# Optimization experiments

Hardware: AMD Instinct MI355X
Metric: run time of the kernel (lower is better)

## Reference

```python
import jax, jax.numpy as jnp
import numpy as np
from jax import lax

TAU = 0.1
DT = 0.001
UNITS = 1024
B, T = 16, 2048


def setup_inputs() -> dict:
    key = jax.random.key(0)
    inputs = jax.random.normal(key, (B, T, UNITS), dtype=jnp.float32)
    level_var = jnp.zeros((1, UNITS), dtype=jnp.float32)
    e = np.exp(-DT / TAU)
    smoothing_init = np.log(e / (1.0 - e)).astype(np.float32)
    smoothing_var = jnp.ones((1, UNITS), dtype=jnp.float32) * smoothing_init
    return {"inputs": inputs, "level_var": level_var, "smoothing_var": smoothing_var}


def reference(inputs, level_var, smoothing_var):
    # inputs: [B, T, U]; level_var, smoothing_var: [1, U]
    s = jax.nn.sigmoid(smoothing_var)  # [1, U]
    level0 = jnp.broadcast_to(level_var, (inputs.shape[0], inputs.shape[2]))  # [B, U]

    def step(level, x_t):
        new = (1.0 - s) * x_t + s * level  # [B, U]
        return new, new

    _, levels = lax.scan(step, level0, jnp.swapaxes(inputs, 0, 1))  # [T, B, U]
    return jnp.swapaxes(levels, 0, 1)  # [B, T, U]
```

## Files before the change

kernel.cpp:

```cpp
#include <hip/hip_runtime.h>


typedef float f32x4 __attribute__((ext_vector_type(4)));

constexpr int B   = 16;
constexpr int T   = 2048;
constexpr int U   = 1024;
constexpr int U4  = U / 4;
constexpr int BU4 = B * U4;

__device__ __forceinline__ float sigmoidf(float x) {
    return 1.0f / (1.0f + __expf(-x));
}

template <int C>
__global__ __launch_bounds__(64) void lowpass_partial(
    const f32x4* __restrict__ in,
    const float* __restrict__ smooth,
    f32x4*       __restrict__ P)
{
    constexpr int L  = T / C;
    constexpr int D1 = 16;
    static_assert(L > D1 && L % D1 == 0, "prefetch");

    const int tid = blockIdx.x * 64 + (int)threadIdx.x;
    const int c   = tid >> 12;
    const int lg  = tid & (BU4 - 1);
    const int b   = lg >> 8;
    const int ug  = lg & (U4 - 1);

    const f32x4 sm = reinterpret_cast<const f32x4*>(smooth)[ug];
    const float s0 = sigmoidf(sm.x), s1 = sigmoidf(sm.y),
                s2 = sigmoidf(sm.z), s3 = sigmoidf(sm.w);
    const float o0 = 1.0f - s0, o1 = 1.0f - s1,
                o2 = 1.0f - s2, o3 = 1.0f - s3;

    const f32x4* __restrict__ ip = in + (b * T + c * L) * U4 + ug;

    float a0 = 0.0f, a1 = 0.0f, a2 = 0.0f, a3 = 0.0f;
    f32x4 buf[D1];
    #pragma unroll
    for (int i = 0; i < D1; ++i) buf[i] = ip[i * U4];

    int t = 0;
    for (; t < L - D1; t += D1) {
        #pragma unroll
        for (int j = 0; j < D1; ++j) {
            f32x4 x = buf[j];
            buf[j] = ip[(t + D1 + j) * U4];
            a0 = fmaf(s0, a0, o0 * x.x);
            a1 = fmaf(s1, a1, o1 * x.y);
            a2 = fmaf(s2, a2, o2 * x.z);
            a3 = fmaf(s3, a3, o3 * x.w);
        }
    }
    #pragma unroll
    for (int j = 0; j < D1; ++j) {
        f32x4 x = buf[j];
        a0 = fmaf(s0, a0, o0 * x.x);
        a1 = fmaf(s1, a1, o1 * x.y);
        a2 = fmaf(s2, a2, o2 * x.z);
        a3 = fmaf(s3, a3, o3 * x.w);
    }
    f32x4 part; part.x = a0; part.y = a1; part.z = a2; part.w = a3;
    P[c * BU4 + lg] = part;
}

template <int C>
__global__ __launch_bounds__(64) void lowpass_scan(
    const f32x4* __restrict__ in,
    const float* __restrict__ level0,
    const float* __restrict__ smooth,
    const f32x4* __restrict__ P,
    f32x4*       __restrict__ out)
{
    constexpr int L    = T / C;
    constexpr int D2   = 8;
    constexpr int LOG2L = 31 - __builtin_clz(L);
    static_assert(L > D2 && L % D2 == 0, "prefetch");
    static_assert((1 << LOG2L) == L, "pow2");

    const int tid = blockIdx.x * 64 + (int)threadIdx.x;
    const int c   = tid >> 12;
    const int lg  = tid & (BU4 - 1);
    const int b   = lg >> 8;
    const int ug  = lg & (U4 - 1);

    const f32x4 sm = reinterpret_cast<const f32x4*>(smooth)[ug];
    const float s0 = sigmoidf(sm.x), s1 = sigmoidf(sm.y),
                s2 = sigmoidf(sm.z), s3 = sigmoidf(sm.w);
    const float o0 = 1.0f - s0, o1 = 1.0f - s1,
                o2 = 1.0f - s2, o3 = 1.0f - s3;

    float sL0 = s0, sL1 = s1, sL2 = s2, sL3 = s3;
    #pragma unroll
    for (int i = 0; i < LOG2L; ++i) {
        sL0 *= sL0; sL1 *= sL1; sL2 *= sL2; sL3 *= sL3;
    }

    const f32x4 l0 = reinterpret_cast<const f32x4*>(level0)[ug];
    float v0 = l0.x, v1 = l0.y, v2 = l0.z, v3 = l0.w;
    for (int i = 0; i < c; ++i) {
        f32x4 p = P[i * BU4 + lg];
        v0 = fmaf(sL0, v0, p.x);
        v1 = fmaf(sL1, v1, p.y);
        v2 = fmaf(sL2, v2, p.z);
        v3 = fmaf(sL3, v3, p.w);
    }

    const int base = (b * T + c * L) * U4 + ug;
    const f32x4* __restrict__ ip = in  + base;
    f32x4*       __restrict__ op = out + base;

    f32x4 buf[D2];
    #pragma unroll
    for (int i = 0; i < D2; ++i) buf[i] = ip[i * U4];

    int t = 0;
    for (; t < L - D2; t += D2) {
        #pragma unroll
        for (int j = 0; j < D2; ++j) {
            f32x4 x = buf[j];
            buf[j] = ip[(t + D2 + j) * U4];
            v0 = fmaf(s0, v0, o0 * x.x);
            v1 = fmaf(s1, v1, o1 * x.y);
            v2 = fmaf(s2, v2, o2 * x.z);
            v3 = fmaf(s3, v3, o3 * x.w);
            f32x4 r; r.x = v0; r.y = v1; r.z = v2; r.w = v3;
            __builtin_nontemporal_store(r, &op[(t + j) * U4]);
        }
    }
    #pragma unroll
    for (int j = 0; j < D2; ++j) {
        f32x4 x = buf[j];
        v0 = fmaf(s0, v0, o0 * x.x);
        v1 = fmaf(s1, v1, o1 * x.y);
        v2 = fmaf(s2, v2, o2 * x.z);
        v3 = fmaf(s3, v3, o3 * x.w);
        f32x4 r; r.x = v0; r.y = v1; r.z = v2; r.w = v3;
        __builtin_nontemporal_store(r, &op[(t + j) * U4]);
    }
}

extern "C" void kernel_launch(void* const* d_in, const int* in_sizes, int n_in,
                              void* d_out, int out_size, void* d_ws, size_t ws_size,
                              hipStream_t stream) {
    const f32x4* in     = (const f32x4*)d_in[0];
    const float* level0 = (const float*)d_in[1];
    const float* smooth = (const float*)d_in[2];
    f32x4* out          = (f32x4*)d_out;
    f32x4* P            = (f32x4*)d_ws;

    dim3 block(64);
    if (ws_size >= (size_t)16 * BU4 * sizeof(f32x4)) {
        constexpr int C = 16;
        dim3 grid(C * BU4 / 64);
        hipLaunchKernelGGL(lowpass_partial<C>, grid, block, 0, stream, in, smooth, P);
        hipLaunchKernelGGL(lowpass_scan<C>,    grid, block, 0, stream, in, level0, smooth, P, out);
    } else {
        constexpr int C = 8;
        dim3 grid(C * BU4 / 64);
        hipLaunchKernelGGL(lowpass_partial<C>, grid, block, 0, stream, in, smooth, P);
        hipLaunchKernelGGL(lowpass_scan<C>,    grid, block, 0, stream, in, level0, smooth, P, out);
    }
}
```

Baseline: 256.0 us.

## Fuse partial and scan passes into single-pass chunked lookback kernel

Replaces the two-kernel chunked scan (partial sums, then rescan) with one kernel. Each block computes its chunk's partial, publishes it with a release flag, then spins on the flags of earlier chunks before rescanning and writing output. This removes a kernel launch boundary, so the rescan of a chunk can overlap with other chunks' partial passes and the input may still be in cache. Chunk count doubles to 32 with 256-thread blocks. The spin-wait relies on earlier blocks being resident or scheduled first, which risks deadlock, and it adds a memset launch.

```diff
diff --git a/kernel.cpp b/kernel.cpp
--- a/kernel.cpp
+++ b/kernel.cpp
@@ -14,91 +14,86 @@
 }
 
 template <int C>
-__global__ __launch_bounds__(64) void lowpass_partial(
+__global__ __launch_bounds__(256, 2) void lowpass_lookback(
     const f32x4* __restrict__ in,
+    const float* __restrict__ level0,
     const float* __restrict__ smooth,
-    f32x4*       __restrict__ P)
+    f32x4*       __restrict__ P,
+    unsigned*    __restrict__ flags,
+    f32x4*       __restrict__ out)
 {
     constexpr int L  = T / C;
-    constexpr int D1 = 16;
-    static_assert(L > D1 && L % D1 == 0, "prefetch");
-
-    const int tid = blockIdx.x * 64 + (int)threadIdx.x;
-    const int c   = tid >> 12;
-    const int lg  = tid & (BU4 - 1);
-    const int b   = lg >> 8;
-    const int ug  = lg & (U4 - 1);
-
-    const f32x4 sm = reinterpret_cast<const f32x4*>(smooth)[ug];
+    constexpr int DA = 16;
+    constexpr int DB = 8;
+    constexpr int LOG2L = 31 - __builtin_clz(L);
+    static_assert(L % DA == 0 && L > DA, "A prefetch");
+    static_assert(L % DB == 0 && L > DB, "B prefetch");
+    static_assert((1 << LOG2L) == L, "pow2");
+
+    const int c   = blockIdx.x >> 4;
+    const int b   = blockIdx.x & 15;
+    const int tid = (int)threadIdx.x;
+    const int lg  = b * U4 + tid;
+
+    const f32x4 sm = reinterpret_cast<const f32x4*>(smooth)[tid];
     const float s0 = sigmoidf(sm.x), s1 = sigmoidf(sm.y),
                 s2 = sigmoidf(sm.z), s3 = sigmoidf(sm.w);
     const float o0 = 1.0f - s0, o1 = 1.0f - s1,
                 o2 = 1.0f - s2, o3 = 1.0f - s3;
 
-    const f32x4* __restrict__ ip = in + (b * T + c * L) * U4 + ug;
+    const int base = (b * T + c * L) * U4 + tid;
+    const f32x4* __restrict__ ip = in + base;
 
     float a0 = 0.0f, a1 = 0.0f, a2 = 0.0f, a3 = 0.0f;
-    f32x4 buf[D1];
-    #pragma unroll
-    for (int i = 0; i < D1; ++i) buf[i] = ip[i * U4];
-
-    int t = 0;
-    for (; t < L - D1; t += D1) {
-        #pragma unroll
-        for (int j = 0; j < D1; ++j) {
-            f32x4 x = buf[j];
-            buf[j] = ip[(t + D1 + j) * U4];
+    {
+        f32x4 buf[DA];
+        #pragma unroll
+        for (int i = 0; i < DA; ++i) buf[i] = ip[i * U4];
+
+        int t = 0;
+        for (; t < L - DA; t += DA) {
+            #pragma unroll
+            for (int j = 0; j < DA; ++j) {
+                f32x4 x = buf[j];
+                buf[j] = ip[(t + DA + j) * U4];
+                a0 = fmaf(s0, a0, o0 * x.x);
+                a1 = fmaf(s1, a1, o1 * x.y);
+                a2 = fmaf(s2, a2, o2 * x.z);
+                a3 = fmaf(s3, a3, o3 * x.w);
+            }
+        }
+        #pragma unroll
+        for (int j = 0; j < DA; ++j) {
+            f32x4 x = buf[j];
             a0 = fmaf(s0, a0, o0 * x.x);
             a1 = fmaf(s1, a1, o1 * x.y);
             a2 = fmaf(s2, a2, o2 * x.z);
             a3 = fmaf(s3, a3, o3 * x.w);
         }
     }
-    #pragma unroll
-    for (int j = 0; j < D1; ++j) {
-        f32x4 x = buf[j];
-        a0 = fmaf(s0, a0, o0 * x.x);
-        a1 = fmaf(s1, a1, o1 * x.y);
-        a2 = fmaf(s2, a2, o2 * x.z);
-        a3 = fmaf(s3, a3, o3 * x.w);
-    }
     f32x4 part; part.x = a0; part.y = a1; part.z = a2; part.w = a3;
     P[c * BU4 + lg] = part;
-}
-
-template <int C>
-__global__ __launch_bounds__(64) void lowpass_scan(
-    const f32x4* __restrict__ in,
-    const float* __restrict__ level0,
-    const float* __restrict__ smooth,
-    const f32x4* __restrict__ P,
-    f32x4*       __restrict__ out)
-{
-    constexpr int L    = T / C;
-    constexpr int D2   = 8;
-    constexpr int LOG2L = 31 - __builtin_clz(L);
-    static_assert(L > D2 && L % D2 == 0, "prefetch");
-    static_assert((1 << LOG2L) == L, "pow2");
-
-    const int tid = blockIdx.x * 64 + (int)threadIdx.x;
-    const int c   = tid >> 12;
-    const int lg  = tid & (BU4 - 1);
-    const int b   = lg >> 8;
-    const int ug  = lg & (U4 - 1);
-
-    const f32x4 sm = reinterpret_cast<const f32x4*>(smooth)[ug];
-    const float s0 = sigmoidf(sm.x), s1 = sigmoidf(sm.y),
-                s2 = sigmoidf(sm.z), s3 = sigmoidf(sm.w);
-    const float o0 = 1.0f - s0, o1 = 1.0f - s1,
-                o2 = 1.0f - s2, o3 = 1.0f - s3;
+
+    __threadfence();
+    __syncthreads();
+    if (tid == 0) {
+        __hip_atomic_store(&flags[blockIdx.x], 1u,
+                           __ATOMIC_RELEASE, __HIP_MEMORY_SCOPE_AGENT);
+    }
+
+    for (int i = 0; i < c; ++i) {
+        while (__hip_atomic_load(&flags[i * 16 + b],
+                                 __ATOMIC_ACQUIRE, __HIP_MEMORY_SCOPE_AGENT) == 0u) {
+            __builtin_amdgcn_s_sleep(1);
+        }
+    }
 
     float sL0 = s0, sL1 = s1, sL2 = s2, sL3 = s3;
     #pragma unroll
     for (int i = 0; i < LOG2L; ++i) {
         sL0 *= sL0; sL1 *= sL1; sL2 *= sL2; sL3 *= sL3;
     }
-
-    const f32x4 l0 = reinterpret_cast<const f32x4*>(level0)[ug];
+    const f32x4 l0 = reinterpret_cast<const f32x4*>(level0)[tid];
     float v0 = l0.x, v1 = l0.y, v2 = l0.z, v3 = l0.w;
     for (int i = 0; i < c; ++i) {
         f32x4 p = P[i * BU4 + lg];
@@ -108,20 +103,17 @@
         v3 = fmaf(sL3, v3, p.w);
     }
 
-    const int base = (b * T + c * L) * U4 + ug;
-    const f32x4* __restrict__ ip = in  + base;
-    f32x4*       __restrict__ op = out + base;
-
-    f32x4 buf[D2];
-    #pragma unroll
-    for (int i = 0; i < D2; ++i) buf[i] = ip[i * U4];
+    f32x4* __restrict__ op = out + base;
+    f32x4 buf[DB];
+    #pragma unroll
+    for (int i = 0; i < DB; ++i) buf[i] = ip[i * U4];
 
     int t = 0;
-    for (; t < L - D2; t += D2) {
-        #pragma unroll
-        for (int j = 0; j < D2; ++j) {
-            f32x4 x = buf[j];
-            buf[j] = ip[(t + D2 + j) * U4];
+    for (; t < L - DB; t += DB) {
+        #pragma unroll
+        for (int j = 0; j < DB; ++j) {
+            f32x4 x = buf[j];
+            buf[j] = ip[(t + DB + j) * U4];
             v0 = fmaf(s0, v0, o0 * x.x);
             v1 = fmaf(s1, v1, o1 * x.y);
             v2 = fmaf(s2, v2, o2 * x.z);
@@ -131,12 +123,117 @@
         }
     }
     #pragma unroll
-    for (int j = 0; j < D2; ++j) {
+    for (int j = 0; j < DB; ++j) {
         f32x4 x = buf[j];
         v0 = fmaf(s0, v0, o0 * x.x);
         v1 = fmaf(s1, v1, o1 * x.y);
         v2 = fmaf(s2, v2, o2 * x.z);
         v3 = fmaf(s3, v3, o3 * x.w);
+        f32x4 r; r.x = v0; r.y = v1; r.z = v2; r.w = v3;
+        __builtin_nontemporal_store(r, &op[(t + j) * U4]);
+    }
+}
+
+template <int C>
+__global__ __launch_bounds__(64) void lowpass_partial(
+    const f32x4* __restrict__ in, const float* __restrict__ smooth,
+    f32x4* __restrict__ P)
+{
+    constexpr int L  = T / C;
+    constexpr int D1 = 16;
+    const int tid = blockIdx.x * 64 + (int)threadIdx.x;
+    const int c  = tid >> 12;
+    const int lg = tid & (BU4 - 1);
+    const int b  = lg >> 8;
+    const int ug = lg & (U4 - 1);
+
+    const f32x4 sm = reinterpret_cast<const f32x4*>(smooth)[ug];
+    const float s0 = sigmoidf(sm.x), s1 = sigmoidf(sm.y),
+                s2 = sigmoidf(sm.z), s3 = sigmoidf(sm.w);
+    const float o0 = 1.0f - s0, o1 = 1.0f - s1,
+                o2 = 1.0f - s2, o3 = 1.0f - s3;
+
+    const f32x4* __restrict__ ip = in + (b * T + c * L) * U4 + ug;
+    float a0 = 0, a1 = 0, a2 = 0, a3 = 0;
+    f32x4 buf[D1];
+    #pragma unroll
+    for (int i = 0; i < D1; ++i) buf[i] = ip[i * U4];
+    int t = 0;
+    for (; t < L - D1; t += D1) {
+        #pragma unroll
+        for (int j = 0; j < D1; ++j) {
+            f32x4 x = buf[j];
+            buf[j] = ip[(t + D1 + j) * U4];
+            a0 = fmaf(s0, a0, o0 * x.x); a1 = fmaf(s1, a1, o1 * x.y);
+            a2 = fmaf(s2, a2, o2 * x.z); a3 = fmaf(s3, a3, o3 * x.w);
+        }
+    }
+    #pragma unroll
+    for (int j = 0; j < D1; ++j) {
+        f32x4 x = buf[j];
+        a0 = fmaf(s0, a0, o0 * x.x); a1 = fmaf(s1, a1, o1 * x.y);
+        a2 = fmaf(s2, a2, o2 * x.z); a3 = fmaf(s3, a3, o3 * x.w);
+    }
+    f32x4 part; part.x = a0; part.y = a1; part.z = a2; part.w = a3;
+    P[c * BU4 + lg] = part;
+}
+
+template <int C>
+__global__ __launch_bounds__(64) void lowpass_scan(
+    const f32x4* __restrict__ in, const float* __restrict__ level0,
+    const float* __restrict__ smooth, const f32x4* __restrict__ P,
+    f32x4* __restrict__ out)
+{
+    constexpr int L  = T / C;
+    constexpr int D2 = 8;
+    constexpr int LOG2L = 31 - __builtin_clz(L);
+    const int tid = blockIdx.x * 64 + (int)threadIdx.x;
+    const int c  = tid >> 12;
+    const int lg = tid & (BU4 - 1);
+    const int b  = lg >> 8;
+    const int ug = lg & (U4 - 1);
+
+    const f32x4 sm = reinterpret_cast<const f32x4*>(smooth)[ug];
+    const float s0 = sigmoidf(sm.x), s1 = sigmoidf(sm.y),
+                s2 = sigmoidf(sm.z), s3 = sigmoidf(sm.w);
+    const float o0 = 1.0f - s0, o1 = 1.0f - s1,
+                o2 = 1.0f - s2, o3 = 1.0f - s3;
+
+    float sL0 = s0, sL1 = s1, sL2 = s2, sL3 = s3;
+    #pragma unroll
+    for (int i = 0; i < LOG2L; ++i) { sL0*=sL0; sL1*=sL1; sL2*=sL2; sL3*=sL3; }
+
+    const f32x4 l0 = reinterpret_cast<const f32x4*>(level0)[ug];
+    float v0 = l0.x, v1 = l0.y, v2 = l0.z, v3 = l0.w;
+    for (int i = 0; i < c; ++i) {
+        f32x4 p = P[i * BU4 + lg];
+        v0 = fmaf(sL0, v0, p.x); v1 = fmaf(sL1, v1, p.y);
+        v2 = fmaf(sL2, v2, p.z); v3 = fmaf(sL3, v3, p.w);
+    }
+
+    const int base = (b * T + c * L) * U4 + ug;
+    const f32x4* __restrict__ ip = in + base;
+    f32x4* __restrict__ op = out + base;
+    f32x4 buf[D2];
+    #pragma unroll
+    for (int i = 0; i < D2; ++i) buf[i] = ip[i * U4];
+    int t = 0;
+    for (; t < L - D2; t += D2) {
+        #pragma unroll
+        for (int j = 0; j < D2; ++j) {
+            f32x4 x = buf[j];
+            buf[j] = ip[(t + D2 + j) * U4];
+            v0 = fmaf(s0, v0, o0 * x.x); v1 = fmaf(s1, v1, o1 * x.y);
+            v2 = fmaf(s2, v2, o2 * x.z); v3 = fmaf(s3, v3, o3 * x.w);
+            f32x4 r; r.x = v0; r.y = v1; r.z = v2; r.w = v3;
+            __builtin_nontemporal_store(r, &op[(t + j) * U4]);
+        }
+    }
+    #pragma unroll
+    for (int j = 0; j < D2; ++j) {
+        f32x4 x = buf[j];
+        v0 = fmaf(s0, v0, o0 * x.x); v1 = fmaf(s1, v1, o1 * x.y);
+        v2 = fmaf(s2, v2, o2 * x.z); v3 = fmaf(s3, v3, o3 * x.w);
         f32x4 r; r.x = v0; r.y = v1; r.z = v2; r.w = v3;
         __builtin_nontemporal_store(r, &op[(t + j) * U4]);
     }
@@ -151,16 +248,26 @@
     f32x4* out          = (f32x4*)d_out;
     f32x4* P            = (f32x4*)d_ws;
 
-    dim3 block(64);
-    if (ws_size >= (size_t)16 * BU4 * sizeof(f32x4)) {
+    const size_t pBytes32 = (size_t)32 * BU4 * sizeof(f32x4);
+    const size_t pBytes16 = (size_t)16 * BU4 * sizeof(f32x4);
+
+    if (ws_size >= pBytes32 + 32 * B * sizeof(unsigned)) {
+        constexpr int C = 32;
+        unsigned* flags = (unsigned*)((char*)d_ws + pBytes32);
+        hipMemsetAsync(flags, 0, C * B * sizeof(unsigned), stream);
+        hipLaunchKernelGGL(lowpass_lookback<C>, dim3(C * B), dim3(256), 0, stream,
+                           in, level0, smooth, P, flags, out);
+    } else if (ws_size >= pBytes16 + 16 * B * sizeof(unsigned)) {
         constexpr int C = 16;
+        unsigned* flags = (unsigned*)((char*)d_ws + pBytes16);
+        hipMemsetAsync(flags, 0, C * B * sizeof(unsigned), stream);
+        hipLaunchKernelGGL(lowpass_lookback<C>, dim3(C * B), dim3(256), 0, stream,
+                           in, level0, smooth, P, flags, out);
+    } else {
+        constexpr int C = 8;
+        dim3 block(64);
         dim3 grid(C * BU4 / 64);
         hipLaunchKernelGGL(lowpass_partial<C>, grid, block, 0, stream, in, smooth, P);
         hipLaunchKernelGGL(lowpass_scan<C>,    grid, block, 0, stream, in, level0, smooth, P, out);
-    } else {
-        constexpr int C = 8;
-        dim3 grid(C * BU4 / 64);
-        hipLaunchKernelGGL(lowpass_partial<C>, grid, block, 0, stream, in, smooth, P);
-        hipLaunchKernelGGL(lowpass_scan<C>,    grid, block, 0, stream, in, level0, smooth, P, out);
-    }
-}
+    }
+}
```

Result: slower. 546.4 us (+113.4%).
